# Optimization experiments

Hardware: AMD Instinct MI355X
Metric: run time of the kernel (lower is better)

Reference implementation:

```python
import jax, jax.numpy as jnp
import numpy as np

VAR0, VAR1 = 0.1, 0.2
THRESHOLD = 0.35
NEGPOS_RATIO = 7
LOW_GT_THRESH = 0.2  # match() filters GT whose best prior IoU < 0.2


def setup_inputs() -> dict:
    key = jax.random.key(0)
    ks = jax.random.split(key, 8)
    B, P, G = 16, 43008, 128
    loc_data = jax.random.normal(ks[0], (B, P, 4), jnp.float32)
    conf_data = jax.random.normal(ks[1], (B, P, 2), jnp.float32)
    landm_data = jax.random.normal(ks[2], (B, P, 10), jnp.float32)
    # priors in cxcywh form, positive sizes
    pc = jax.random.uniform(ks[3], (P, 2), jnp.float32)
    pwh = jax.random.uniform(ks[4], (P, 2), jnp.float32, minval=0.02, maxval=0.32)
    priors = jnp.concatenate([pc, pwh], axis=1)
    # targets: valid xyxy boxes + 10 landmark coords + label (face=1)
    ctr = jax.random.uniform(ks[5], (B, G, 2), jnp.float32, minval=0.2, maxval=0.8)
    wh = jax.random.uniform(ks[6], (B, G, 2), jnp.float32, minval=0.05, maxval=0.3)
    boxes = jnp.concatenate([ctr - wh / 2, ctr + wh / 2], axis=-1)
    landms = jax.random.uniform(ks[7], (B, G, 10), jnp.float32)
    labels = jnp.ones((B, G, 1), jnp.float32)
    targets = jnp.concatenate([boxes, landms, labels], axis=-1)
    return {"loc_data": loc_data, "conf_data": conf_data, "landm_data": landm_data,
            "priors": priors, "targets": targets}


def point_form(priors):
    return jnp.concatenate([priors[:, :2] - priors[:, 2:] / 2,
                            priors[:, :2] + priors[:, 2:] / 2], axis=1)


def jaccard(a, b):  # a: [G,4] xyxy, b: [P,4] xyxy -> [G,P]
    lt = jnp.maximum(a[:, None, :2], b[None, :, :2])
    rb = jnp.minimum(a[:, None, 2:], b[None, :, 2:])
    wh = jnp.clip(rb - lt, 0.0)
    inter = wh[..., 0] * wh[..., 1]
    area_a = (a[:, 2] - a[:, 0]) * (a[:, 3] - a[:, 1])
    area_b = (b[:, 2] - b[:, 0]) * (b[:, 3] - b[:, 1])
    return inter / (area_a[:, None] + area_b[None, :] - inter)


def encode(matched, priors):  # matched xyxy [P,4], priors cxcywh [P,4]
    g_cxcy = (matched[:, :2] + matched[:, 2:]) / 2 - priors[:, :2]
    g_cxcy = g_cxcy / (VAR0 * priors[:, 2:])
    g_wh = jnp.log((matched[:, 2:] - matched[:, :2]) / priors[:, 2:]) / VAR1
    return jnp.concatenate([g_cxcy, g_wh], axis=1)


def encode_landm(matched, priors):  # matched [P,10], priors [P,4]
    m = matched.reshape(-1, 5, 2)
    g = (m - priors[:, None, :2]) / (VAR0 * priors[:, None, 2:])
    return g.reshape(-1, 10)


def match_one(truths, labels, landms, priors):
    G = truths.shape[0]
    overlaps = jaccard(truths, point_form(priors))  # [G, P]
    best_prior_overlap = overlaps.max(axis=1)       # [G]
    best_prior_idx = overlaps.argmax(axis=1)        # [G]
    valid = best_prior_overlap >= LOW_GT_THRESH
    any_valid = jnp.any(valid)
    best_truth_overlap = overlaps.max(axis=0)       # [P]
    best_truth_idx = overlaps.argmax(axis=0)        # [P]
    # index_fill_(0, best_prior_idx_filter, 2): ensure each valid GT keeps its best prior
    fill_val = jnp.where(valid, 2.0, best_truth_overlap[best_prior_idx])
    best_truth_overlap = best_truth_overlap.at[best_prior_idx].set(fill_val)
    # best_truth_idx[best_prior_idx[j]] = j for all j
    best_truth_idx = best_truth_idx.at[best_prior_idx].set(jnp.arange(G))
    matches = truths[best_truth_idx]                       # [P,4]
    conf = labels[best_truth_idx].astype(jnp.int32)        # [P]
    conf = jnp.where(best_truth_overlap < THRESHOLD, 0, conf)
    conf = jnp.where(any_valid, conf, 0)  # no valid GT -> all background
    loc = encode(matches, priors)
    landm = encode_landm(landms[best_truth_idx], priors)
    return loc, conf, landm


def smooth_l1(x):
    ax = jnp.abs(x)
    return jnp.where(ax < 1.0, 0.5 * ax * ax, ax - 0.5)


def reference(loc_data, conf_data, landm_data, priors, targets):
    truths = targets[..., :4]
    landms = targets[..., 4:14]
    labels = targets[..., 14]
    loc_t, conf_t, landm_t = jax.vmap(
        lambda t, l, lm: match_one(t, l, lm, priors))(truths, labels, landms)

    # landmark loss over positives
    pos1 = conf_t > 0
    N1 = jnp.maximum(pos1.sum().astype(jnp.float32), 1.0)
    loss_landm = jnp.sum(smooth_l1(landm_data - landm_t) * pos1[..., None])

    # localization loss over positives
    pos = conf_t != 0
    num_pos = pos.sum(axis=1, keepdims=True)  # [B,1]
    loss_l = jnp.sum(smooth_l1(loc_data - loc_t) * pos[..., None])

    # hard negative mining on per-prior CE loss
    lse = jax.scipy.special.logsumexp(conf_data, axis=-1)  # [B,P]
    gathered = jnp.take_along_axis(conf_data, conf_t[..., None], axis=-1)[..., 0]
    ce_all = lse - gathered                                # [B,P] per-prior CE
    mine = jnp.where(pos, 0.0, ce_all)
    loss_idx = jnp.argsort(-mine, axis=1)
    idx_rank = jnp.argsort(loss_idx, axis=1)
    num_neg = jnp.clip(NEGPOS_RATIO * num_pos, None, pos.shape[1] - 1)
    neg = idx_rank < num_neg
    sel = pos | neg
    loss_c = jnp.sum(jnp.where(sel, ce_all, 0.0))

    N = jnp.maximum(num_pos.sum().astype(jnp.float32), 1.0)
    return loss_l / N, loss_c / N, loss_landm / N1
```

## Files before the change

kernel.cpp:

```cpp
#include <hip/hip_runtime.h>
#include <stdint.h>


#define GC 8
#define PPI 4

__device__ __forceinline__ float sl1(float x) {
  float a = fabsf(x);
  return a < 1.f ? 0.5f * a * a : a - 0.5f;
}

__device__ __forceinline__ double dwave(double v) {
#pragma unroll
  for (int o = 32; o; o >>= 1) v += __shfl_down(v, o);
  return v;
}

__global__ __launch_bounds__(256) void k_match(
    const float* __restrict__ priors, const float* __restrict__ targets,
    float* __restrict__ bto, int* __restrict__ bti,
    unsigned long long* __restrict__ bp, int P, int G, int NIOU, int PTI,
    int NGC, int PC) {
  int tid = threadIdx.x;
  __shared__ float4 sgt[128];
  __shared__ float sga[128];
  __shared__ unsigned long long sred[GC * 256];

  if ((int)blockIdx.x < NIOU) {
    int b = blockIdx.x / PTI, tile = blockIdx.x % PTI;
    int base = tile * (256 * PPI);
    for (int g = tid; g < G; g += 256) {
      const float* t = targets + ((size_t)b * G + g) * 15;
      float x1 = t[0], y1 = t[1], x2 = t[2], y2 = t[3];
      sgt[g] = make_float4(x1, y1, x2, y2);
      sga[g] = (x2 - x1) * (y2 - y1);
    }
    __syncthreads();

    float px1[PPI], py1[PPI], px2[PPI], py2[PPI], pa[PPI];
    float bi[PPI], sb[PPI];
    int bidx[PPI];
#pragma unroll
    for (int k = 0; k < PPI; ++k) {
      int p = base + tid + k * 256;
      int pl = p < P ? p : P - 1;
      float4 pr = ((const float4*)priors)[pl];
      px1[k] = pr.x - pr.z * 0.5f; py1[k] = pr.y - pr.w * 0.5f;
      px2[k] = pr.x + pr.z * 0.5f; py2[k] = pr.y + pr.w * 0.5f;
      pa[k] = pr.z * pr.w;
      bi[k] = 0.f; sb[k] = 1.f; bidx[k] = 0;
    }

    for (int g = 0; g < G; g += 2) {
      float4 T0 = sgt[g];
      float4 T1 = sgt[g + 1];
      float A0 = sga[g];
      float A1 = sga[g + 1];
#pragma unroll
      for (int k = 0; k < PPI; ++k) {
        {
          float iw = fminf(T0.z, px2[k]) - fmaxf(T0.x, px1[k]);
          float ih = fminf(T0.w, py2[k]) - fmaxf(T0.y, py1[k]);
          float inter = fmaxf(iw, 0.f) * fmaxf(ih, 0.f);
          float S = A0 + pa[k];
          if (inter * sb[k] > bi[k] * S) { bi[k] = inter; sb[k] = S; bidx[k] = g; }
        }
        {
          float iw = fminf(T1.z, px2[k]) - fmaxf(T1.x, px1[k]);
          float ih = fminf(T1.w, py2[k]) - fmaxf(T1.y, py1[k]);
          float inter = fmaxf(iw, 0.f) * fmaxf(ih, 0.f);
          float S = A1 + pa[k];
          if (inter * sb[k] > bi[k] * S) { bi[k] = inter; sb[k] = S; bidx[k] = g + 1; }
        }
      }
    }
#pragma unroll
    for (int k = 0; k < PPI; ++k) {
      int p = base + tid + k * 256;
      if (p < P) {
        bto[(size_t)b * P + p] = bi[k] / (sb[k] - bi[k]);
        bti[(size_t)b * P + p] = bidx[k];
      }
    }
  } else {
    int bc = blockIdx.x - NIOU;
    int pc = bc % PC;
    int gcb = (bc / PC) % NGC;
    int b = bc / (PC * NGC);
    int g0 = gcb * GC;

    if (tid < GC) {
      int g = g0 + tid;
      float4 v = make_float4(0.f, 0.f, 0.f, 0.f);
      if (g < G) {
        const float* t = targets + ((size_t)b * G + g) * 15;
        v = make_float4(t[0], t[1], t[2], t[3]);
      }
      sgt[tid] = v;
    }
    __syncthreads();

    float gx1[GC], gy1[GC], gx2[GC], gy2[GC], ga[GC];
#pragma unroll
    for (int j = 0; j < GC; ++j) {
      float4 T = sgt[j];
      gx1[j] = T.x; gy1[j] = T.y; gx2[j] = T.z; gy2[j] = T.w;
      ga[j] = (T.z - T.x) * (T.w - T.y);
    }

    int chunk = (P + PC - 1) / PC;
    int ps = pc * chunk;
    int pe = ps + chunk; if (pe > P) pe = P;
    int count = pe - ps;

    float bi[GC], sb[GC];
    unsigned bpp[GC];
#pragma unroll
    for (int j = 0; j < GC; ++j) { bi[j] = 0.f; sb[j] = 1.f; bpp[j] = (unsigned)(ps + tid); }

    for (int i = tid; i < count; i += 512) {
      int p0 = ps + i;
      int i1 = i + 256;
      int p1 = (i1 < count) ? ps + i1 : p0;
      float4 q0 = ((const float4*)priors)[p0];
      float4 q1 = ((const float4*)priors)[p1];
      float ax1 = q0.x - q0.z * 0.5f, ay1 = q0.y - q0.w * 0.5f;
      float ax2 = q0.x + q0.z * 0.5f, ay2 = q0.y + q0.w * 0.5f;
      float aa = q0.z * q0.w;
      float bx1 = q1.x - q1.z * 0.5f, by1 = q1.y - q1.w * 0.5f;
      float bx2 = q1.x + q1.z * 0.5f, by2 = q1.y + q1.w * 0.5f;
      float ba = q1.z * q1.w;
#pragma unroll
      for (int j = 0; j < GC; ++j) {
        {
          float iw = fminf(gx2[j], ax2) - fmaxf(gx1[j], ax1);
          float ih = fminf(gy2[j], ay2) - fmaxf(gy1[j], ay1);
          float inter = fmaxf(iw, 0.f) * fmaxf(ih, 0.f);
          float S = ga[j] + aa;
          if (inter * sb[j] > bi[j] * S) { bi[j] = inter; sb[j] = S; bpp[j] = (unsigned)p0; }
        }
        {
          float iw = fminf(gx2[j], bx2) - fmaxf(gx1[j], bx1);
          float ih = fminf(gy2[j], by2) - fmaxf(gy1[j], by1);
          float inter = fmaxf(iw, 0.f) * fmaxf(ih, 0.f);
          float S = ga[j] + ba;
          if (inter * sb[j] > bi[j] * S) { bi[j] = inter; sb[j] = S; bpp[j] = (unsigned)p1; }
        }
      }
    }

#pragma unroll
    for (int j = 0; j < GC; ++j) {
      float iou = bi[j] / (sb[j] - bi[j]);
      unsigned long long pk =
          ((unsigned long long)__float_as_uint(iou) << 32) | (unsigned)(~bpp[j]);
      sred[j * 256 + tid] = pk;
    }
    __syncthreads();
    {
      int j = tid >> 5, s = tid & 31;
      unsigned long long m = sred[j * 256 + s];
#pragma unroll
      for (int t = 1; t < 8; ++t) {
        unsigned long long v = sred[j * 256 + s + t * 32];
        if (v > m) m = v;
      }
      __syncthreads();
      sred[j * 256 + s] = m;
    }
    __syncthreads();
    if (tid < GC) {
      unsigned long long m = sred[tid * 256];
      for (int s = 1; s < 32; ++s) {
        unsigned long long v = sred[tid * 256 + s];
        if (v > m) m = v;
      }
      int g = g0 + tid;
      if (g < G) atomicMax(&bp[(size_t)b * G + g], m);
    }
  }
}

__global__ __launch_bounds__(256) void k_main(
    const float* __restrict__ loc, const float* __restrict__ conf,
    const float* __restrict__ lm, const float* __restrict__ priors,
    const float* __restrict__ targets, const float* __restrict__ bto,
    const int* __restrict__ bti, const unsigned long long* __restrict__ bp,
    float* __restrict__ mine, unsigned* __restrict__ h1,
    double* __restrict__ pll, double* __restrict__ pllm,
    double* __restrict__ plc, double* __restrict__ msum,
    int* __restrict__ pnp, int P, int G, int PT) {
  int b = blockIdx.x / PT, tile = blockIdx.x % PT;
  int tid = threadIdx.x;
  int base = tile * 256;
  int p = base + tid;

  __shared__ float st[128 * 15];
  __shared__ unsigned hist[1024];
  __shared__ unsigned long long sbp[128];
  __shared__ short forced[256];
  __shared__ int s_any;
  __shared__ double rs[16];
  __shared__ int ri[4];

  for (int i = tid; i < G * 15; i += 256) st[i] = targets[(size_t)b * G * 15 + i];
  for (int i = tid; i < 1024; i += 256) hist[i] = 0;
  if (tid < G) sbp[tid] = bp[(size_t)b * G + tid];
  forced[tid] = -1;
  if (tid == 0) s_any = 0;
  __syncthreads();

  if (tid < G) {
    unsigned long long m = sbp[tid];
    unsigned pp = ~(unsigned)m;
    float val = __uint_as_float((unsigned)(m >> 32));
    if (val >= 0.2f) s_any = 1;
    bool win = true;
    for (int g2 = tid + 1; g2 < G; ++g2)
      if ((~(unsigned)sbp[g2]) == pp) { win = false; break; }
    int local = (int)pp - base;
    if (win && local >= 0 && local < 256)
      forced[local] = (short)((tid << 1) | (val >= 0.2f ? 1 : 0));
  }
  __syncthreads();

  double ll = 0, llm = 0, lc = 0, ms = 0;
  int np = 0;
  if (p < P) {
    size_t idx = (size_t)b * P + p;
    int av = s_any;
    float ov = bto[idx];
    int ti = bti[idx];
    int f = forced[tid];
    if (f >= 0) {
      ti = f >> 1;
      if (f & 1) ov = 2.0f;
    }
    bool pos = av && (ov >= 0.35f);

    float2 c = ((const float2*)conf)[idx];
    float mx = fmaxf(c.x, c.y);
    float lse = mx + logf(expf(c.x - mx) + expf(c.y - mx));
    float ce = lse - (pos ? c.y : c.x);
    float mv = pos ? 0.f : ce;
    mine[idx] = mv;
    ms = (double)mv;
    atomicAdd(&hist[__float_as_uint(mv) >> 21], 1u);

    if (pos) {
      np = 1;
      lc = (double)ce;
      float4 pr = ((const float4*)priors)[p];
      const float* t = st + ti * 15;
      float dx = 0.1f * pr.z, dy = 0.1f * pr.w;
      float gx = ((t[0] + t[2]) * 0.5f - pr.x) / dx;
      float gy = ((t[1] + t[3]) * 0.5f - pr.y) / dy;
      float gw = logf((t[2] - t[0]) / pr.z) * 5.0f;
      float gh = logf((t[3] - t[1]) / pr.w) * 5.0f;
      float4 ld = ((const float4*)loc)[idx];
      ll = (double)(sl1(ld.x - gx) + sl1(ld.y - gy) + sl1(ld.z - gw) +
                    sl1(ld.w - gh));
      const float2* lmd = (const float2*)lm + idx * 5;
      float s = 0.f;
#pragma unroll
      for (int j = 0; j < 5; ++j) {
        float2 lv = lmd[j];
        float ex = (t[4 + 2 * j] - pr.x) / dx;
        float ey = (t[5 + 2 * j] - pr.y) / dy;
        s += sl1(lv.x - ex) + sl1(lv.y - ey);
      }
      llm = (double)s;
    }
  }

  ll = dwave(ll);
  llm = dwave(llm);
  lc = dwave(lc);
  ms = dwave(ms);
#pragma unroll
  for (int o = 32; o; o >>= 1) np += __shfl_down(np, o);
  int lane = tid & 63, wid = tid >> 6;
  if (lane == 0) {
    rs[wid] = ll; rs[4 + wid] = llm; rs[8 + wid] = lc; rs[12 + wid] = ms;
    ri[wid] = np;
  }
  __syncthreads();
  if (tid == 0) {
    pll[blockIdx.x] = rs[0] + rs[1] + rs[2] + rs[3];
    pllm[blockIdx.x] = rs[4] + rs[5] + rs[6] + rs[7];
    plc[blockIdx.x] = rs[8] + rs[9] + rs[10] + rs[11];
    msum[blockIdx.x] = rs[12] + rs[13] + rs[14] + rs[15];
    pnp[blockIdx.x] = ri[0] + ri[1] + ri[2] + ri[3];
  }
  for (int i = tid; i < 1024; i += 256)
    if (hist[i]) atomicAdd(&h1[(size_t)b * 1024 + i], hist[i]);
}

__global__ __launch_bounds__(256) void k_tail(
    const unsigned* __restrict__ h1, const int* __restrict__ pnp,
    const double* __restrict__ msum, const float* __restrict__ mine,
    int* __restrict__ num_pos, double* __restrict__ pfs_b, int P, int PT) {
  int b = blockIdx.x, tid = threadIdx.x;
  __shared__ int sn[256];
  __shared__ double sm[256];
  __shared__ unsigned hs[2048];
  __shared__ unsigned S[256];
  __shared__ int spf1, sk1, spf21, sk2;
  __shared__ unsigned stb;
  __shared__ double stie;
  __shared__ double rs[4];

  int n = 0;
  double m = 0;
  for (int i = tid; i < PT; i += 256) { n += pnp[b * PT + i]; m += msum[b * PT + i]; }
  sn[tid] = n; sm[tid] = m;
  __syncthreads();
  for (int off = 128; off; off >>= 1) {
    if (tid < off) { sn[tid] += sn[tid + off]; sm[tid] += sm[tid + off]; }
    __syncthreads();
  }
  int npos = sn[0];
  if (tid == 0) num_pos[b] = npos;

  long long k = 7LL * (long long)npos;
  long long cap = P - 1;
  if (k <= 0) return;
  if (k >= cap) {
    if (tid == 0) pfs_b[b] = sm[0];
    return;
  }

  {
    const unsigned* h = h1 + (size_t)b * 1024;
    unsigned p0 = h[tid * 4], p1 = h[tid * 4 + 1], p2 = h[tid * 4 + 2],
             p3 = h[tid * 4 + 3];
    S[tid] = p0 + p1 + p2 + p3;
    __syncthreads();
    for (int off = 1; off < 256; off <<= 1) {
      unsigned add = (tid + off < 256) ? S[tid + off] : 0;
      __syncthreads();
      S[tid] += add;
      __syncthreads();
    }
    int cnt = __syncthreads_count((long long)S[tid] >= k);
    int seg = cnt - 1;
    if (tid == seg) {
      long long cum = (seg + 1 < 256) ? (long long)S[seg + 1] : 0;
      unsigned hv[4] = {p0, p1, p2, p3};
      int bin = seg * 4;
      for (int j = 3; j >= 0; --j) {
        if (cum + hv[j] >= k) { bin = seg * 4 + j; break; }
        cum += hv[j];
      }
      spf1 = bin;
      sk1 = (int)(k - cum);
    }
  }
  __syncthreads();
  int pf = spf1;
  const float* mrow = mine + (size_t)b * P;

  for (int i = tid; i < 2048; i += 256) hs[i] = 0;
  __syncthreads();
  for (int i = tid; i < P; i += 256) {
    unsigned bits = __float_as_uint(mrow[i]);
    if ((int)(bits >> 21) == pf) atomicAdd(&hs[(bits >> 10) & 2047], 1u);
  }
  __syncthreads();
  {
    unsigned hv[8];
    unsigned s = 0;
#pragma unroll
    for (int j = 0; j < 8; ++j) { hv[j] = hs[tid * 8 + j]; s += hv[j]; }
    S[tid] = s;
    __syncthreads();
    for (int off = 1; off < 256; off <<= 1) {
      unsigned add = (tid + off < 256) ? S[tid + off] : 0;
      __syncthreads();
      S[tid] += add;
      __syncthreads();
    }
    long long kk = (long long)sk1;
    int cnt = __syncthreads_count((long long)S[tid] >= kk);
    int seg = cnt - 1;
    if (tid == seg) {
      long long cum = (seg + 1 < 256) ? (long long)S[seg + 1] : 0;
      int bin = seg * 8;
      for (int j = 7; j >= 0; --j) {
        if (cum + hv[j] >= kk) { bin = seg * 8 + j; break; }
        cum += hv[j];
      }
      spf21 = (pf << 11) | bin;
      sk2 = (int)(kk - cum);
    }
  }
  __syncthreads();
  int pf21 = spf21;

  for (int i = tid; i < 1024; i += 256) hs[i] = 0;
  __syncthreads();
  for (int i = tid; i < P; i += 256) {
    unsigned bits = __float_as_uint(mrow[i]);
    if ((int)(bits >> 10) == pf21) atomicAdd(&hs[bits & 1023], 1u);
  }
  __syncthreads();
  {
    unsigned p0 = hs[tid * 4], p1 = hs[tid * 4 + 1], p2 = hs[tid * 4 + 2],
             p3 = hs[tid * 4 + 3];
    S[tid] = p0 + p1 + p2 + p3;
    __syncthreads();
    for (int off = 1; off < 256; off <<= 1) {
      unsigned add = (tid + off < 256) ? S[tid + off] : 0;
      __syncthreads();
      S[tid] += add;
      __syncthreads();
    }
    long long kk = (long long)sk2;
    int cnt = __syncthreads_count((long long)S[tid] >= kk);
    int seg = cnt - 1;
    if (tid == seg) {
      long long cum = (seg + 1 < 256) ? (long long)S[seg + 1] : 0;
      unsigned hv[4] = {p0, p1, p2, p3};
      int bin = seg * 4;
      for (int j = 3; j >= 0; --j) {
        if (cum + hv[j] >= kk) { bin = seg * 4 + j; break; }
        cum += hv[j];
      }
      unsigned tb = ((unsigned)pf21 << 10) | (unsigned)bin;
      stb = tb;
      stie = (double)(kk - cum) * (double)__uint_as_float(tb);
    }
  }
  __syncthreads();

  unsigned tb = stb;
  double v = 0.0;
  for (int i = tid; i < P; i += 256) {
    unsigned bits = __float_as_uint(mrow[i]);
    if (bits > tb) v += (double)__uint_as_float(bits);
  }
  v = dwave(v);
  int lane = tid & 63, wid = tid >> 6;
  if (lane == 0) rs[wid] = v;
  __syncthreads();
  if (tid == 0) pfs_b[b] = rs[0] + rs[1] + rs[2] + rs[3] + stie;
}

__global__ __launch_bounds__(256) void k_fin(
    const double* __restrict__ pll, const double* __restrict__ pllm,
    const double* __restrict__ plc, const double* __restrict__ pfs_b,
    const int* __restrict__ num_pos, float* __restrict__ out, int NBm, int B) {
  int tid = threadIdx.x;
  double a = 0, c = 0, d = 0, f = 0, n = 0;
  for (int i = tid; i < NBm; i += 256) { a += pll[i]; c += pllm[i]; d += plc[i]; }
  for (int i = tid; i < B; i += 256) { f += pfs_b[i]; n += (double)num_pos[i]; }
  a = dwave(a); c = dwave(c); d = dwave(d); f = dwave(f); n = dwave(n);
  __shared__ double rs[5 * 4];
  int lane = tid & 63, wid = tid >> 6;
  if (lane == 0) {
    rs[wid] = a; rs[4 + wid] = c; rs[8 + wid] = d;
    rs[12 + wid] = f; rs[16 + wid] = n;
  }
  __syncthreads();
  if (tid == 0) {
    double A = rs[0] + rs[1] + rs[2] + rs[3];
    double C = rs[4] + rs[5] + rs[6] + rs[7];
    double D = rs[8] + rs[9] + rs[10] + rs[11];
    double F = rs[12] + rs[13] + rs[14] + rs[15];
    double N = rs[16] + rs[17] + rs[18] + rs[19];
    if (N < 1.0) N = 1.0;
    out[0] = (float)(A / N);
    out[1] = (float)((D + F) / N);
    out[2] = (float)(C / N);
  }
}

extern "C" void kernel_launch(void* const* d_in, const int* in_sizes, int n_in,
                              void* d_out, int out_size, void* d_ws,
                              size_t ws_size, hipStream_t stream) {
  const float* loc = (const float*)d_in[0];
  const float* conf = (const float*)d_in[1];
  const float* lm = (const float*)d_in[2];
  const float* priors = (const float*)d_in[3];
  const float* targets = (const float*)d_in[4];

  int P = in_sizes[3] / 4;
  int B = in_sizes[0] / (4 * P);
  int G = in_sizes[4] / (15 * B);
  int PT = (P + 255) / 256;
  int PTI = (P + 256 * PPI - 1) / (256 * PPI);
  int NBm = B * PT;
  int NGC = (G + GC - 1) / GC;
  int PC = 8;
  int NIOU = B * PTI;
  int NBP = B * NGC * PC;

  char* w = (char*)d_ws;
  size_t off = 0;
  unsigned long long* bp = (unsigned long long*)(w + off);
  off += (size_t)B * G * 8;
  double* pfs_b = (double*)(w + off);
  off += (size_t)B * 8;
  int* num_pos = (int*)(w + off);
  off += (size_t)B * 4;
  off = (off + 7) & ~(size_t)7;
  unsigned* h1 = (unsigned*)(w + off);
  off += (size_t)B * 1024 * 4;
  size_t clear_bytes = off;
  off = (off + 255) & ~(size_t)255;
  float* bto = (float*)(w + off);
  off += (size_t)B * P * 4;
  int* bti = (int*)(w + off);
  off += (size_t)B * P * 4;
  float* mine = (float*)(w + off);
  off += (size_t)B * P * 4;
  double* pll = (double*)(w + off);
  off += (size_t)NBm * 8;
  double* pllm = (double*)(w + off);
  off += (size_t)NBm * 8;
  double* plc = (double*)(w + off);
  off += (size_t)NBm * 8;
  double* msum = (double*)(w + off);
  off += (size_t)NBm * 8;
  int* pnp = (int*)(w + off);
  off += (size_t)NBm * 4;

  hipMemsetAsync(d_ws, 0, clear_bytes, stream);

  k_match<<<NIOU + NBP, 256, 0, stream>>>(priors, targets, bto, bti, bp, P, G,
                                          NIOU, PTI, NGC, PC);
  k_main<<<B * PT, 256, 0, stream>>>(loc, conf, lm, priors, targets, bto, bti,
                                     bp, mine, h1, pll, pllm, plc, msum, pnp,
                                     P, G, PT);
  k_tail<<<B, 256, 0, stream>>>(h1, pnp, msum, mine, num_pos, pfs_b, P, PT);
  k_fin<<<1, 256, 0, stream>>>(pll, pllm, plc, pfs_b, num_pos, (float*)d_out,
                               NBm, B);
}
```

Baseline: 196.3 us.

## Unroll IoU loops, add scatter kernel for forced matches, widen tail to 1024 threads

```diff
diff --git a/kernel.cpp b/kernel.cpp
--- a/kernel.cpp
+++ b/kernel.cpp
@@ -51,29 +51,27 @@
       bi[k] = 0.f; sb[k] = 1.f; bidx[k] = 0;
     }
 
-    for (int g = 0; g < G; g += 2) {
-      float4 T0 = sgt[g];
-      float4 T1 = sgt[g + 1];
-      float A0 = sga[g];
-      float A1 = sga[g + 1];
+#define IOU_BODY(T, A, GG)                                                 \
+  {                                                                        \
+    float iw = fminf(T.z, px2[k]) - fmaxf(T.x, px1[k]);                    \
+    float ih = fminf(T.w, py2[k]) - fmaxf(T.y, py1[k]);                    \
+    float inter = fmaxf(iw, 0.f) * ih;        \
+    float S = A + pa[k];                                                   \
+    if (inter * sb[k] > bi[k] * S) { bi[k] = inter; sb[k] = S; bidx[k] = GG; } \
+  }
+
+    for (int g = 0; g < G; g += 4) {
+      float4 T0 = sgt[g], T1 = sgt[g + 1], T2 = sgt[g + 2], T3 = sgt[g + 3];
+      float A0 = sga[g], A1 = sga[g + 1], A2 = sga[g + 2], A3 = sga[g + 3];
 #pragma unroll
       for (int k = 0; k < PPI; ++k) {
-        {
-          float iw = fminf(T0.z, px2[k]) - fmaxf(T0.x, px1[k]);
-          float ih = fminf(T0.w, py2[k]) - fmaxf(T0.y, py1[k]);
-          float inter = fmaxf(iw, 0.f) * fmaxf(ih, 0.f);
-          float S = A0 + pa[k];
-          if (inter * sb[k] > bi[k] * S) { bi[k] = inter; sb[k] = S; bidx[k] = g; }
-        }
-        {
-          float iw = fminf(T1.z, px2[k]) - fmaxf(T1.x, px1[k]);
-          float ih = fminf(T1.w, py2[k]) - fmaxf(T1.y, py1[k]);
-          float inter = fmaxf(iw, 0.f) * fmaxf(ih, 0.f);
-          float S = A1 + pa[k];
-          if (inter * sb[k] > bi[k] * S) { bi[k] = inter; sb[k] = S; bidx[k] = g + 1; }
-        }
-      }
-    }
+        IOU_BODY(T0, A0, g)
+        IOU_BODY(T1, A1, g + 1)
+        IOU_BODY(T2, A2, g + 2)
+        IOU_BODY(T3, A3, g + 3)
+      }
+    }
+#undef IOU_BODY
 #pragma unroll
     for (int k = 0; k < PPI; ++k) {
       int p = base + tid + k * 256;
@@ -118,36 +116,46 @@
 #pragma unroll
     for (int j = 0; j < GC; ++j) { bi[j] = 0.f; sb[j] = 1.f; bpp[j] = (unsigned)(ps + tid); }
 
-    for (int i = tid; i < count; i += 512) {
+#define BP_BODY(X1, Y1, X2, Y2, AR, PP)                                     \
+  {                                                                         \
+    float iw = fminf(gx2[j], X2) - fmaxf(gx1[j], X1);                       \
+    float ih = fminf(gy2[j], Y2) - fmaxf(gy1[j], Y1);                       \
+    float inter = fmaxf(iw, 0.f) * ih;                                      \
+    float S = ga[j] + AR;                                                   \
+    if (inter * sb[j] > bi[j] * S) { bi[j] = inter; sb[j] = S; bpp[j] = (unsigned)PP; } \
+  }
+
+    for (int i = tid; i < count; i += 1024) {
       int p0 = ps + i;
-      int i1 = i + 256;
+      int i1 = i + 256, i2 = i + 512, i3 = i + 768;
       int p1 = (i1 < count) ? ps + i1 : p0;
+      int p2 = (i2 < count) ? ps + i2 : p0;
+      int p3 = (i3 < count) ? ps + i3 : p0;
       float4 q0 = ((const float4*)priors)[p0];
       float4 q1 = ((const float4*)priors)[p1];
+      float4 q2 = ((const float4*)priors)[p2];
+      float4 q3 = ((const float4*)priors)[p3];
       float ax1 = q0.x - q0.z * 0.5f, ay1 = q0.y - q0.w * 0.5f;
       float ax2 = q0.x + q0.z * 0.5f, ay2 = q0.y + q0.w * 0.5f;
       float aa = q0.z * q0.w;
       float bx1 = q1.x - q1.z * 0.5f, by1 = q1.y - q1.w * 0.5f;
       float bx2 = q1.x + q1.z * 0.5f, by2 = q1.y + q1.w * 0.5f;
       float ba = q1.z * q1.w;
+      float cx1 = q2.x - q2.z * 0.5f, cy1 = q2.y - q2.w * 0.5f;
+      float cx2 = q2.x + q2.z * 0.5f, cy2 = q2.y + q2.w * 0.5f;
+      float ca = q2.z * q2.w;
+      float dx1 = q3.x - q3.z * 0.5f, dy1 = q3.y - q3.w * 0.5f;
+      float dx2 = q3.x + q3.z * 0.5f, dy2 = q3.y + q3.w * 0.5f;
+      float da = q3.z * q3.w;
 #pragma unroll
       for (int j = 0; j < GC; ++j) {
-        {
-          float iw = fminf(gx2[j], ax2) - fmaxf(gx1[j], ax1);
-          float ih = fminf(gy2[j], ay2) - fmaxf(gy1[j], ay1);
-          float inter = fmaxf(iw, 0.f) * fmaxf(ih, 0.f);
-          float S = ga[j] + aa;
-          if (inter * sb[j] > bi[j] * S) { bi[j] = inter; sb[j] = S; bpp[j] = (unsigned)p0; }
-        }
-        {
-          float iw = fminf(gx2[j], bx2) - fmaxf(gx1[j], bx1);
-          float ih = fminf(gy2[j], by2) - fmaxf(gy1[j], by1);
-          float inter = fmaxf(iw, 0.f) * fmaxf(ih, 0.f);
-          float S = ga[j] + ba;
-          if (inter * sb[j] > bi[j] * S) { bi[j] = inter; sb[j] = S; bpp[j] = (unsigned)p1; }
-        }
-      }
-    }
+        BP_BODY(ax1, ay1, ax2, ay2, aa, p0)
+        BP_BODY(bx1, by1, bx2, by2, ba, p1)
+        BP_BODY(cx1, cy1, cx2, cy2, ca, p2)
+        BP_BODY(dx1, dy1, dx2, dy2, da, p3)
+      }
+    }
+#undef BP_BODY
 
 #pragma unroll
     for (int j = 0; j < GC; ++j) {
@@ -181,61 +189,63 @@
   }
 }
 
+__global__ void k_scatter(const unsigned long long* __restrict__ bp,
+                          float* __restrict__ bto, int* __restrict__ bti,
+                          int* __restrict__ anyv, int P, int G) {
+  int b = blockIdx.x, g = threadIdx.x;
+  __shared__ unsigned spp[128];
+  __shared__ int s_any;
+  if (g == 0) s_any = 0;
+  __syncthreads();
+  unsigned long long m = bp[(size_t)b * G + g];
+  unsigned pp = ~(unsigned)m;
+  float val = __uint_as_float((unsigned)(m >> 32));
+  bool ok = (m != 0ULL);
+  float oldv = 0.f;
+  if (ok) oldv = bto[(size_t)b * P + pp];
+  spp[g] = ok ? pp : 0xFFFFFFFFu;
+  if (ok && val >= 0.2f) s_any = 1;
+  __syncthreads();
+  bool win = ok;
+  for (int g2 = g + 1; g2 < G; ++g2)
+    if (spp[g2] == pp) win = false;
+  if (win) {
+    bto[(size_t)b * P + pp] = (val >= 0.2f) ? 2.0f : oldv;
+    bti[(size_t)b * P + pp] = g;
+  }
+  __syncthreads();
+  if (g == 0) anyv[b] = s_any;
+}
+
 __global__ __launch_bounds__(256) void k_main(
     const float* __restrict__ loc, const float* __restrict__ conf,
     const float* __restrict__ lm, const float* __restrict__ priors,
     const float* __restrict__ targets, const float* __restrict__ bto,
-    const int* __restrict__ bti, const unsigned long long* __restrict__ bp,
+    const int* __restrict__ bti, const int* __restrict__ anyv,
     float* __restrict__ mine, unsigned* __restrict__ h1,
     double* __restrict__ pll, double* __restrict__ pllm,
     double* __restrict__ plc, double* __restrict__ msum,
     int* __restrict__ pnp, int P, int G, int PT) {
   int b = blockIdx.x / PT, tile = blockIdx.x % PT;
   int tid = threadIdx.x;
-  int base = tile * 256;
-  int p = base + tid;
+  int p = tile * 256 + tid;
 
   __shared__ float st[128 * 15];
   __shared__ unsigned hist[1024];
-  __shared__ unsigned long long sbp[128];
-  __shared__ short forced[256];
-  __shared__ int s_any;
   __shared__ double rs[16];
   __shared__ int ri[4];
 
   for (int i = tid; i < G * 15; i += 256) st[i] = targets[(size_t)b * G * 15 + i];
   for (int i = tid; i < 1024; i += 256) hist[i] = 0;
-  if (tid < G) sbp[tid] = bp[(size_t)b * G + tid];
-  forced[tid] = -1;
-  if (tid == 0) s_any = 0;
-  __syncthreads();
-
-  if (tid < G) {
-    unsigned long long m = sbp[tid];
-    unsigned pp = ~(unsigned)m;
-    float val = __uint_as_float((unsigned)(m >> 32));
-    if (val >= 0.2f) s_any = 1;
-    bool win = true;
-    for (int g2 = tid + 1; g2 < G; ++g2)
-      if ((~(unsigned)sbp[g2]) == pp) { win = false; break; }
-    int local = (int)pp - base;
-    if (win && local >= 0 && local < 256)
-      forced[local] = (short)((tid << 1) | (val >= 0.2f ? 1 : 0));
-  }
   __syncthreads();
 
   double ll = 0, llm = 0, lc = 0, ms = 0;
   int np = 0;
   if (p < P) {
     size_t idx = (size_t)b * P + p;
-    int av = s_any;
+    int av = anyv[b];
     float ov = bto[idx];
     int ti = bti[idx];
-    int f = forced[tid];
-    if (f >= 0) {
-      ti = f >> 1;
-      if (f & 1) ov = 2.0f;
-    }
     bool pos = av && (ov >= 0.35f);
 
     float2 c = ((const float2*)conf)[idx];
@@ -296,26 +306,26 @@
     if (hist[i]) atomicAdd(&h1[(size_t)b * 1024 + i], hist[i]);
 }
 
-__global__ __launch_bounds__(256) void k_tail(
+__global__ __launch_bounds__(1024) void k_tail(
     const unsigned* __restrict__ h1, const int* __restrict__ pnp,
     const double* __restrict__ msum, const float* __restrict__ mine,
     int* __restrict__ num_pos, double* __restrict__ pfs_b, int P, int PT) {
   int b = blockIdx.x, tid = threadIdx.x;
-  __shared__ int sn[256];
-  __shared__ double sm[256];
+  __shared__ double sm[1024];
+  __shared__ int sn[1024];
+  __shared__ unsigned S[1024];
   __shared__ unsigned hs[2048];
-  __shared__ unsigned S[256];
   __shared__ int spf1, sk1, spf21, sk2;
   __shared__ unsigned stb;
   __shared__ double stie;
-  __shared__ double rs[4];
+  __shared__ double rs[16];
 
   int n = 0;
   double m = 0;
-  for (int i = tid; i < PT; i += 256) { n += pnp[b * PT + i]; m += msum[b * PT + i]; }
+  for (int i = tid; i < PT; i += 1024) { n += pnp[b * PT + i]; m += msum[b * PT + i]; }
   sn[tid] = n; sm[tid] = m;
   __syncthreads();
-  for (int off = 128; off; off >>= 1) {
+  for (int off = 512; off; off >>= 1) {
     if (tid < off) { sn[tid] += sn[tid + off]; sm[tid] += sm[tid + off]; }
     __syncthreads();
   }
@@ -330,14 +340,14 @@
     return;
   }
 
+  const float* mrow = mine + (size_t)b * P;
+
   {
-    const unsigned* h = h1 + (size_t)b * 1024;
-    unsigned p0 = h[tid * 4], p1 = h[tid * 4 + 1], p2 = h[tid * 4 + 2],
-             p3 = h[tid * 4 + 3];
-    S[tid] = p0 + p1 + p2 + p3;
-    __syncthreads();
-    for (int off = 1; off < 256; off <<= 1) {
-      unsigned add = (tid + off < 256) ? S[tid + off] : 0;
+    unsigned own = h1[(size_t)b * 1024 + tid];
+    S[tid] = own;
+    __syncthreads();
+    for (int off = 1; off < 1024; off <<= 1) {
+      unsigned add = (tid + off < 1024) ? S[tid + off] : 0;
       __syncthreads();
       S[tid] += add;
       __syncthreads();
@@ -345,37 +355,35 @@
     int cnt = __syncthreads_count((long long)S[tid] >= k);
     int seg = cnt - 1;
     if (tid == seg) {
-      long long cum = (seg + 1 < 256) ? (long long)S[seg + 1] : 0;
-      unsigned hv[4] = {p0, p1, p2, p3};
-      int bin = seg * 4;
-      for (int j = 3; j >= 0; --j) {
-        if (cum + hv[j] >= k) { bin = seg * 4 + j; break; }
-        cum += hv[j];
-      }
-      spf1 = bin;
+      long long cum = (seg + 1 < 1024) ? (long long)S[seg + 1] : 0;
+      spf1 = seg;
       sk1 = (int)(k - cum);
     }
   }
   __syncthreads();
   int pf = spf1;
-  const float* mrow = mine + (size_t)b * P;
-
-  for (int i = tid; i < 2048; i += 256) hs[i] = 0;
-  __syncthreads();
-  for (int i = tid; i < P; i += 256) {
-    unsigned bits = __float_as_uint(mrow[i]);
-    if ((int)(bits >> 21) == pf) atomicAdd(&hs[(bits >> 10) & 2047], 1u);
+
+  hs[tid] = 0; hs[tid + 1024] = 0;
+  __syncthreads();
+  for (int base = 0; base < P; base += 4096) {
+    int i0 = base + tid;
+    int i1 = i0 + 1024, i2 = i0 + 2048, i3 = i0 + 3072;
+    unsigned b0 = (i0 < P) ? __float_as_uint(mrow[i0]) : 0u;
+    unsigned b1 = (i1 < P) ? __float_as_uint(mrow[i1]) : 0u;
+    unsigned b2 = (i2 < P) ? __float_as_uint(mrow[i2]) : 0u;
+    unsigned b3 = (i3 < P) ? __float_as_uint(mrow[i3]) : 0u;
+    if (i0 < P && (int)(b0 >> 21) == pf) atomicAdd(&hs[(b0 >> 10) & 2047], 1u);
+    if (i1 < P && (int)(b1 >> 21) == pf) atomicAdd(&hs[(b1 >> 10) & 2047], 1u);
+    if (i2 < P && (int)(b2 >> 21) == pf) atomicAdd(&hs[(b2 >> 10) & 2047], 1u);
+    if (i3 < P && (int)(b3 >> 21) == pf) atomicAdd(&hs[(b3 >> 10) & 2047], 1u);
   }
   __syncthreads();
   {
-    unsigned hv[8];
-    unsigned s = 0;
-#pragma unroll
-    for (int j = 0; j < 8; ++j) { hv[j] = hs[tid * 8 + j]; s += hv[j]; }
-    S[tid] = s;
-    __syncthreads();
-    for (int off = 1; off < 256; off <<= 1) {
-      unsigned add = (tid + off < 256) ? S[tid + off] : 0;
+    unsigned h0 = hs[tid * 2], h1v = hs[tid * 2 + 1];
+    S[tid] = h0 + h1v;
+    __syncthreads();
+    for (int off = 1; off < 1024; off <<= 1) {
+      unsigned add = (tid + off < 1024) ? S[tid + off] : 0;
       __syncthreads();
       S[tid] += add;
       __syncthreads();
@@ -384,12 +392,10 @@
     int cnt = __syncthreads_count((long long)S[tid] >= kk);
     int seg = cnt - 1;
     if (tid == seg) {
-      long long cum = (seg + 1 < 256) ? (long long)S[seg + 1] : 0;
-      int bin = seg * 8;
-      for (int j = 7; j >= 0; --j) {
-        if (cum + hv[j] >= kk) { bin = seg * 8 + j; break; }
-        cum += hv[j];
-      }
+      long long cum = (seg + 1 < 1024) ? (long long)S[seg + 1] : 0;
+      int bin = seg * 2;
+      if (cum + h1v >= kk) bin = seg * 2 + 1;
+      else cum += h1v;
       spf21 = (pf << 11) | bin;
       sk2 = (int)(kk - cum);
     }
@@ -397,20 +403,27 @@
   __syncthreads();
   int pf21 = spf21;
 
-  for (int i = tid; i < 1024; i += 256) hs[i] = 0;
-  __syncthreads();
-  for (int i = tid; i < P; i += 256) {
-    unsigned bits = __float_as_uint(mrow[i]);
-    if ((int)(bits >> 10) == pf21) atomicAdd(&hs[bits & 1023], 1u);
+  hs[tid] = 0;
+  __syncthreads();
+  for (int base = 0; base < P; base += 4096) {
+    int i0 = base + tid;
+    int i1 = i0 + 1024, i2 = i0 + 2048, i3 = i0 + 3072;
+    unsigned b0 = (i0 < P) ? __float_as_uint(mrow[i0]) : 0u;
+    unsigned b1 = (i1 < P) ? __float_as_uint(mrow[i1]) : 0u;
+    unsigned b2 = (i2 < P) ? __float_as_uint(mrow[i2]) : 0u;
+    unsigned b3 = (i3 < P) ? __float_as_uint(mrow[i3]) : 0u;
+    if (i0 < P && (int)(b0 >> 10) == pf21) atomicAdd(&hs[b0 & 1023], 1u);
+    if (i1 < P && (int)(b1 >> 10) == pf21) atomicAdd(&hs[b1 & 1023], 1u);
+    if (i2 < P && (int)(b2 >> 10) == pf21) atomicAdd(&hs[b2 & 1023], 1u);
+    if (i3 < P && (int)(b3 >> 10) == pf21) atomicAdd(&hs[b3 & 1023], 1u);
   }
   __syncthreads();
   {
-    unsigned p0 = hs[tid * 4], p1 = hs[tid * 4 + 1], p2 = hs[tid * 4 + 2],
-             p3 = hs[tid * 4 + 3];
-    S[tid] = p0 + p1 + p2 + p3;
-    __syncthreads();
-    for (int off = 1; off < 256; off <<= 1) {
-      unsigned add = (tid + off < 256) ? S[tid + off] : 0;
+    unsigned own = hs[tid];
+    S[tid] = own;
+    __syncthreads();
+    for (int off = 1; off < 1024; off <<= 1) {
+      unsigned add = (tid + off < 1024) ? S[tid + off] : 0;
       __syncthreads();
       S[tid] += add;
       __syncthreads();
@@ -419,14 +432,8 @@
     int cnt = __syncthreads_count((long long)S[tid] >= kk);
     int seg = cnt - 1;
     if (tid == seg) {
-      long long cum = (seg + 1 < 256) ? (long long)S[seg + 1] : 0;
-      unsigned hv[4] = {p0, p1, p2, p3};
-      int bin = seg * 4;
-      for (int j = 3; j >= 0; --j) {
-        if (cum + hv[j] >= kk) { bin = seg * 4 + j; break; }
-        cum += hv[j];
-      }
-      unsigned tb = ((unsigned)pf21 << 10) | (unsigned)bin;
+      long long cum = (seg + 1 < 1024) ? (long long)S[seg + 1] : 0;
+      unsigned tb = ((unsigned)pf21 << 10) | (unsigned)seg;
       stb = tb;
       stie = (double)(kk - cum) * (double)__uint_as_float(tb);
     }
@@ -435,15 +442,27 @@
 
   unsigned tb = stb;
   double v = 0.0;
-  for (int i = tid; i < P; i += 256) {
-    unsigned bits = __float_as_uint(mrow[i]);
-    if (bits > tb) v += (double)__uint_as_float(bits);
+  for (int base = 0; base < P; base += 4096) {
+    int i0 = base + tid;
+    int i1 = i0 + 1024, i2 = i0 + 2048, i3 = i0 + 3072;
+    unsigned b0 = (i0 < P) ? __float_as_uint(mrow[i0]) : 0u;
+    unsigned b1 = (i1 < P) ? __float_as_uint(mrow[i1]) : 0u;
+    unsigned b2 = (i2 < P) ? __float_as_uint(mrow[i2]) : 0u;
+    unsigned b3 = (i3 < P) ? __float_as_uint(mrow[i3]) : 0u;
+    if (b0 > tb) v += (double)__uint_as_float(b0);
+    if (b1 > tb) v += (double)__uint_as_float(b1);
+    if (b2 > tb) v += (double)__uint_as_float(b2);
+    if (b3 > tb) v += (double)__uint_as_float(b3);
   }
   v = dwave(v);
   int lane = tid & 63, wid = tid >> 6;
   if (lane == 0) rs[wid] = v;
   __syncthreads();
-  if (tid == 0) pfs_b[b] = rs[0] + rs[1] + rs[2] + rs[3] + stie;
+  if (tid == 0) {
+    double t = 0;
+    for (int i = 0; i < 16; ++i) t += rs[i];
+    pfs_b[b] = t + stie;
+  }
 }
 
 __global__ __launch_bounds__(256) void k_fin(
@@ -501,9 +520,10 @@
   off += (size_t)B * G * 8;
   double* pfs_b = (double*)(w + off);
   off += (size_t)B * 8;
-  int* num_pos = (int*)(w + off);
-  off += (size_t)B * 4;
-  off = (off + 7) & ~(size_t)7;
+  int* ctrl = (int*)(w + off);
+  off += (size_t)(2 * B) * 4;
+  int* anyv = ctrl;
+  int* num_pos = ctrl + B;
   unsigned* h1 = (unsigned*)(w + off);
   off += (size_t)B * 1024 * 4;
   size_t clear_bytes = off;
@@ -529,10 +549,11 @@
 
   k_match<<<NIOU + NBP, 256, 0, stream>>>(priors, targets, bto, bti, bp, P, G,
                                           NIOU, PTI, NGC, PC);
+  k_scatter<<<B, G, 0, stream>>>(bp, bto, bti, anyv, P, G);
   k_main<<<B * PT, 256, 0, stream>>>(loc, conf, lm, priors, targets, bto, bti,
-                                     bp, mine, h1, pll, pllm, plc, msum, pnp,
+                                     anyv, mine, h1, pll, pllm, plc, msum, pnp,
                                      P, G, PT);
-  k_tail<<<B, 256, 0, stream>>>(h1, pnp, msum, mine, num_pos, pfs_b, P, PT);
+  k_tail<<<B, 1024, 0, stream>>>(h1, pnp, msum, mine, num_pos, pfs_b, P, PT);
   k_fin<<<1, 256, 0, stream>>>(pll, pllm, plc, pfs_b, num_pos, (float*)d_out,
                                NBm, B);
 }
```

Result: faster. 178.8 us (-9.0%).
